# Kernel optimization log

Measured on AMD Instinct MI355X. Metric: run time of the kernel, lower is better.

Reference implementation:

```python
import jax, jax.numpy as jnp
import numpy as np
from jax import lax

DN = ('NCHW', 'OIHW', 'NCHW')

def _pconv(x, mask, w, b):
    # Partial conv: conv(masked x) rescaled by K/valid_count; mask_next = valid>0.
    C = x.shape[1]
    k = w.shape[2]
    p = k // 2
    K = C * k * k
    xm = x * mask  # mask broadcasts over channels (== repeat in torch code)
    xp = jnp.pad(xm, ((0, 0), (0, 0), (p, p), (p, p)))  # zeros, as in F.pad value=0
    y = lax.conv_general_dilated(xp, w, (1, 1), 'VALID', dimension_numbers=DN)
    # mask padded with 1.0 (as in the torch module), summed over kxk window
    mp = jnp.pad(mask, ((0, 0), (0, 0), (p, p), (p, p)), constant_values=1.0)
    ones_k = jnp.ones((1, 1, k, k), x.dtype)
    msum = lax.conv_general_dilated(mp, ones_k, (1, 1), 'VALID', dimension_numbers=DN)
    valid = C * msum  # [N,1,H,W] = sum over all K unfold rows
    scale = K / jnp.maximum(valid, 1.0)
    y = y * scale + b[None, :, None, None]
    no_valid = valid <= 0.0
    y = jnp.where(no_valid, 0.0, y)
    mask_next = (~no_valid).astype(x.dtype)
    return y, mask_next

def _bn_relu(x, gamma, beta, eps=1e-5):
    # training-mode BatchNorm2d: per-batch biased stats over (N,H,W)
    mu = jnp.mean(x, axis=(0, 2, 3), keepdims=True)
    var = jnp.var(x, axis=(0, 2, 3), keepdims=True)
    xn = (x - mu) * lax.rsqrt(var + eps)
    return jax.nn.relu(xn * gamma[None, :, None, None] + beta[None, :, None, None])

def _pool21(x):
    # MaxPool2d(kernel=(2,1), stride=(2,1))
    N, C, H, W = x.shape
    return x.reshape(N, C, H // 2, 2, W).max(axis=3)

def setup_inputs() -> dict:
    key = jax.random.key(0)
    ks = iter(jax.random.split(key, 32))
    base = 80
    def kaiming(k, shape):
        fan_in = shape[1] * shape[2] * shape[3]
        return jax.random.normal(k, shape, jnp.float32) * np.sqrt(2.0 / fan_in)
    def lin(k, out, inp):
        bound = 1.0 / np.sqrt(inp)
        kw, kb = jax.random.split(k)
        W = jax.random.uniform(kw, (out, inp), jnp.float32, -bound, bound)
        b = jax.random.uniform(kb, (out,), jnp.float32, -bound, bound)
        return W, b
    x = jax.random.normal(next(ks), (16, 2, 256, 128), jnp.float32)
    d = {'x': x}
    chans = [(1, base), (base, 2 * base), (2 * base, 4 * base), (4 * base, 8 * base)]
    for i, (ci, co) in enumerate(chans, 1):
        d[f'w{i}'] = kaiming(next(ks), (co, ci, 3, 3))
        d[f'b{i}'] = jnp.zeros((co,), jnp.float32)
        d[f'g{i}'] = jnp.ones((co,), jnp.float32)
        d[f'be{i}'] = jnp.zeros((co,), jnp.float32)
    d['fw1'], d['fb1'] = lin(next(ks), 256, 8 * base)
    d['fw2'], d['fb2'] = lin(next(ks), 128, 256)
    d['hw'], d['hb'] = lin(next(ks), 1, 128)
    return d

def reference(x, w1, b1, g1, be1, w2, b2, g2, be2, w3, b3, g3, be3,
              w4, b4, g4, be4, fw1, fb1, fw2, fb2, hw, hb):
    data = x[:, 0:1, :, :]
    mask = jnp.clip(x[:, 1:2, :, :], 0.0, 1.0)
    h, m = data, mask
    for w, b, g, be in ((w1, b1, g1, be1), (w2, b2, g2, be2),
                        (w3, b3, g3, be3), (w4, b4, g4, be4)):
        h, m = _pconv(h, m, w, b)
        h = _bn_relu(h, g, be)
        h = _pool21(h)
        m = _pool21(m)
    feat = jnp.mean(h, axis=(2, 3))  # GAP -> [N, 8*base]
    z = jax.nn.relu(feat @ fw1.T + fb1)
    z = jax.nn.relu(z @ fw2.T + fb2)  # dropout = identity (eval)
    return jax.nn.sigmoid(z @ hw.T + hb)[:, 0]
```

## Files before the change

### kernel.cpp

```cpp
#include <hip/hip_runtime.h>
#include <math.h>

#define NB 16
#define WD 128

typedef __bf16 bf16_t;
typedef __bf16 bf16x8 __attribute__((ext_vector_type(8)));
typedef __bf16 bf16x4 __attribute__((ext_vector_type(4)));
typedef float f32x4 __attribute__((ext_vector_type(4)));

__device__ inline float rowsum16(float v) {
  int t;
  t = __builtin_amdgcn_update_dpp(0, __float_as_int(v), 0x111, 0xf, 0xf, true);
  v += __int_as_float(t);
  t = __builtin_amdgcn_update_dpp(0, __float_as_int(v), 0x112, 0xf, 0xf, true);
  v += __int_as_float(t);
  t = __builtin_amdgcn_update_dpp(0, __float_as_int(v), 0x114, 0xf, 0xf, true);
  v += __int_as_float(t);
  t = __builtin_amdgcn_update_dpp(0, __float_as_int(v), 0x118, 0xf, 0xf, true);
  v += __int_as_float(t);
  return v;
}

__global__ void zero_k(float* __restrict__ p, int n) {
  int i = blockIdx.x * 256 + threadIdx.x;
  if (i < n) p[i] = 0.f;
}

__global__ void zb_k(bf16_t* __restrict__ out, int Hp, int NCB) {
  int trow = NB * 2 * NCB * 576;
  int tcol = NB * Hp * NCB * 8;
  int i = blockIdx.x * 256 + threadIdx.x;
  bf16x8 z = (bf16x8)(bf16_t)0.f;
  if (i < trow) {
    int e = i % 576;
    int t = i / 576;
    int cb = t % NCB;
    t /= NCB;
    int rsel = t & 1;
    int n = t >> 1;
    int row = rsel ? (Hp + 1) : 0;
    *(bf16x8*)&out[(((size_t)n * (Hp + 2) + row) * NCB + cb) * 4608 + e * 8] = z;
  } else if (i < trow + tcol) {
    int k = i - trow;
    int j = k & 7;
    int t = k >> 3;
    int cb = t % NCB;
    t /= NCB;
    int row = (t % Hp) + 1;
    int n = t / Hp;
    size_t base = (((size_t)n * (Hp + 2) + row) * NCB + cb) * 4608;
    size_t off = (j < 4) ? (size_t)(j * 128) : (size_t)(4096 + (j - 4) * 128 + 8);
    *(bf16x8*)&out[base + off] = z;
  }
}

__global__ void split_k(const float* __restrict__ x, float* __restrict__ data,
                        float* __restrict__ mask) {
  const int HW = 256 * 128;
  int i = blockIdx.x * 256 + threadIdx.x;
  if (i >= NB * HW) return;
  int n = i / HW, rem = i % HW;
  data[i] = x[(size_t)(n * 2) * HW + rem];
  float mv = x[(size_t)(n * 2 + 1) * HW + rem];
  mask[i] = fminf(fmaxf(mv, 0.f), 1.f);
}

__global__ void maskscale2_k(const float* __restrict__ m, float* __restrict__ scale,
                             float* __restrict__ mnext, float* __restrict__ mpool,
                             int H, float Ci) {
  int Hp = H / 2;
  int i = blockIdx.x * 256 + threadIdx.x;
  int tot = NB * Hp * WD;
  if (i >= tot) return;
  int x = i % WD;
  int t = i / WD;
  int yo = t % Hp;
  int n = t / Hp;
  const float* mn_ = m + (size_t)n * H * WD;
  float mx[2];
#pragma unroll
  for (int r = 0; r < 2; ++r) {
    int y = 2 * yo + r;
    float s = 0.f;
#pragma unroll
    for (int dy = -1; dy <= 1; dy++) {
      int yy = y + dy;
#pragma unroll
      for (int dx = -1; dx <= 1; dx++) {
        int xx = x + dx;
        float v = 1.0f;
        if (yy >= 0 && yy < H && xx >= 0 && xx < WD) v = mn_[yy * WD + xx];
        s += v;
      }
    }
    float valid = Ci * s;
    int p = (n * H + y) * WD + x;
    scale[p] = (9.0f * Ci) / fmaxf(valid, 1.0f);
    float mnx = (valid <= 0.0f) ? 0.f : 1.f;
    mnext[p] = mnx;
    mx[r] = mnx;
  }
  mpool[((size_t)n * Hp + yo) * WD + x] = fmaxf(mx[0], mx[1]);
}

__global__ void pconv1_k(const float* __restrict__ data, const float* __restrict__ mask,
                         const float* __restrict__ w, const float* __restrict__ b,
                         const float* __restrict__ scale, const float* __restrict__ mnext,
                         bf16_t* __restrict__ y) {
  __shared__ float ws[720];
  __shared__ float bs[80];
  for (int i = threadIdx.x; i < 720; i += 256) ws[i] = w[i];
  if (threadIdx.x < 80) bs[threadIdx.x] = b[threadIdx.x];
  __syncthreads();
  const int H = 256;
  int p = blockIdx.x * 256 + threadIdx.x;
  int x = p % WD;
  int t = p / WD;
  int yy = t % H;
  int n = t / H;
  const float* dn = data + (size_t)n * H * WD;
  const float* mn = mask + (size_t)n * H * WD;
  float v[9];
#pragma unroll
  for (int dy = 0; dy < 3; dy++) {
    int yv = yy - 1 + dy;
#pragma unroll
    for (int dx = 0; dx < 3; dx++) {
      int xv = x - 1 + dx;
      float u = 0.f;
      if (yv >= 0 && yv < H && xv >= 0 && xv < WD)
        u = dn[yv * WD + xv] * mn[yv * WD + xv];
      v[dy * 3 + dx] = u;
    }
  }
  float sc = scale[p], mx = mnext[p];
  bf16_t* yp = y + (size_t)p * 80;
#pragma unroll
  for (int c8 = 0; c8 < 10; ++c8) {
    bf16x8 o;
#pragma unroll
    for (int j = 0; j < 8; ++j) {
      int co = c8 * 8 + j;
      float s = 0.f;
#pragma unroll
      for (int tt = 0; tt < 9; ++tt) s += ws[co * 9 + tt] * v[tt];
      o[j] = (bf16_t)((s * sc + bs[co]) * mx);
    }
    *(bf16x8*)(yp + c8 * 8) = o;
  }
}

__global__ __launch_bounds__(320) void bnstats_g(const bf16_t* __restrict__ y,
                                                 float* __restrict__ sums, int nc8) {
  const int ITER = 64;
  const int tid = threadIdx.x;
  const int C = nc8 * 8;
  float s[8], q[8];
#pragma unroll
  for (int j = 0; j < 8; ++j) { s[j] = 0.f; q[j] = 0.f; }
  size_t base = (size_t)blockIdx.x * 320 * ITER;
  for (int k = 0; k < ITER; ++k) {
    size_t chunk = base + (size_t)k * 320 + tid;
    bf16x8 v = *(const bf16x8*)(y + chunk * 8);
#pragma unroll
    for (int j = 0; j < 8; ++j) {
      float f = (float)v[j];
      s[j] += f;
      q[j] += f * f;
    }
  }
  __shared__ float red[320][8];
  const int rows = 320 / nc8;
  float ssum[2], qsum[2];
#pragma unroll
  for (int j = 0; j < 8; ++j) red[tid][j] = s[j];
  __syncthreads();
  {
    int idx = 0;
    for (int c = tid; c < C; c += 320, ++idx) {
      int c8 = c >> 3, j = c & 7;
      float acc = 0.f;
      for (int i = 0; i < rows; ++i) acc += red[c8 + nc8 * i][j];
      ssum[idx] = acc;
    }
  }
  __syncthreads();
#pragma unroll
  for (int j = 0; j < 8; ++j) red[tid][j] = q[j];
  __syncthreads();
  {
    int idx = 0;
    for (int c = tid; c < C; c += 320, ++idx) {
      int c8 = c >> 3, j = c & 7;
      float acc = 0.f;
      for (int i = 0; i < rows; ++i) acc += red[c8 + nc8 * i][j];
      qsum[idx] = acc;
      atomicAdd(&sums[c], ssum[idx]);
      atomicAdd(&sums[C + c], qsum[idx]);
    }
  }
}

__global__ void wtrans_k(const float* __restrict__ w, bf16_t* __restrict__ wt2,
                         int Ci, int Co, int NCB, int Co_pad) {
  int idx = blockIdx.x * 256 + threadIdx.x;
  int total = 9 * NCB * Co_pad * 32;
  if (idx >= total) return;
  int j = idx & 7;
  int rest = idx >> 3;
  int co = rest % Co_pad;
  int rest2 = rest / Co_pad;
  int g = rest2 & 3;
  int rest3 = rest2 >> 2;
  int cb = rest3 % NCB;
  int tap = rest3 / NCB;
  int ci = cb * 32 + g * 8 + j;
  float v = 0.f;
  if (co < Co && ci < Ci) v = w[((size_t)co * Ci + ci) * 9 + tap];
  wt2[idx] = (bf16_t)v;
}

#define PROWS 2048
#define PCO 640
template <int MF>
__global__ __launch_bounds__(256, 2) void convmfma_t(
    const bf16_t* __restrict__ xmT, const bf16_t* __restrict__ wt2,
    const float* __restrict__ bias, const float* __restrict__ scale,
    const float* __restrict__ mnext, bf16_t* __restrict__ y,
    float* __restrict__ part, int H, int NCB, int Co, int Cop, int coOff) {
  __shared__ bf16_t Bb[2][4][4608];
  const int tid = threadIdx.x;
  const int lane = tid & 63;
  const int wave = tid >> 6;
  const int wm = wave >> 1;
  const int wn = wave & 1;
  const int g = lane >> 4;
  const int ln = lane & 15;
  constexpr int TILE = MF * 32;
  constexpr int EPS = TILE + 8;
  constexpr int NCO8 = TILE / 8;

  const int gx = gridDim.x;
  const int nwg = gx * (int)gridDim.y;
  const int orig = (int)blockIdx.y * gx + (int)blockIdx.x;
  const int wg = (orig & 7) * (nwg >> 3) + (orig >> 3);
  const int coTile = coOff + (wg % gx) * TILE;
  const int bx = wg / gx;
  const int Hh = H >> 1;
  const int n = bx / Hh, y0 = (bx % Hh) * 2;

  f32x4 acc[MF][8];
#pragma unroll
  for (int mf = 0; mf < MF; mf++)
#pragma unroll
    for (int nf = 0; nf < 8; nf++) acc[mf][nf] = (f32x4)(0.f);

  const size_t cbStride = 4608;
  const size_t rowStrideG = (size_t)NCB * cbStride;
  const size_t gRow0 = ((size_t)n * (H + 2) + y0) * rowStrideG;
  const size_t laneOff = (size_t)lane * 8;

  const size_t tapStrideA = (size_t)NCB * 4 * Cop * 8;
  const size_t cbStrideA = (size_t)4 * Cop * 8;
  const bf16_t* aLane = wt2 + ((size_t)g * Cop + coTile + wm * (MF * 16) + ln) * 8;

  int offdx[3];
#pragma unroll
  for (int dx = 0; dx < 3; ++dx) {
    int cx = ln + dx;
    offdx[dx] = ((cx & 15) * 8) + ((cx >> 4) * 512) + g * 128;
  }

  {
    const bf16_t* bsrc = xmT + gRow0;
    for (int c = wave; c < 36; c += 4) {
      int row = c / 9, chk = c - row * 9;
      __builtin_amdgcn_global_load_lds(
          (const __attribute__((address_space(1))) void*)(
              bsrc + (size_t)row * rowStrideG + chk * 512 + laneOff),
          (__attribute__((address_space(3))) void*)(&Bb[0][row][chk * 512]), 16, 0, 0);
    }
  }
  __syncthreads();

  int cur = 0;
  for (int cb = 0; cb < NCB; ++cb) {
    if (cb + 1 < NCB) {
      const bf16_t* bsrc = xmT + gRow0 + (size_t)(cb + 1) * cbStride;
      for (int c = wave; c < 36; c += 4) {
        int row = c / 9, chk = c - row * 9;
        __builtin_amdgcn_global_load_lds(
            (const __attribute__((address_space(1))) void*)(
                bsrc + (size_t)row * rowStrideG + chk * 512 + laneOff),
            (__attribute__((address_space(3))) void*)(&Bb[cur ^ 1][row][chk * 512]), 16,
            0, 0);
      }
    }
    const bf16_t* aCb = aLane + (size_t)cb * cbStrideA;
#pragma unroll
    for (int dy = 0; dy < 3; ++dy) {
      const bf16_t* brow = &Bb[cur][wn + dy][0];
#pragma unroll
      for (int dx = 0; dx < 3; ++dx) {
        const bf16_t* aTap = aCb + (size_t)(dy * 3 + dx) * tapStrideA;
        bf16x8 a[MF];
#pragma unroll
        for (int mf = 0; mf < MF; ++mf) a[mf] = *(const bf16x8*)(aTap + mf * 128);
        const bf16_t* bb = brow + offdx[dx];
#pragma unroll
        for (int nf = 0; nf < 8; ++nf) {
          bf16x8 b = *(const bf16x8*)(bb + nf * 512);
#pragma unroll
          for (int mf = 0; mf < MF; ++mf)
            acc[mf][nf] =
                __builtin_amdgcn_mfma_f32_16x16x32_bf16(a[mf], b, acc[mf][nf], 0, 0, 0);
        }
      }
    }
    __syncthreads();
    cur ^= 1;
  }

  const int yrowW = y0 + wn;
  const int pixBaseW = (n * H + yrowW) * WD;
  float scl[8], msk[8];
#pragma unroll
  for (int nf = 0; nf < 8; ++nf) {
    int x = nf * 16 + ln;
    scl[nf] = scale[pixBaseW + x];
    msk[nf] = mnext[pixBaseW + x];
  }
  float sA[4 * MF], qA[4 * MF];
#pragma unroll
  for (int i = 0; i < 4 * MF; ++i) { sA[i] = 0.f; qA[i] = 0.f; }
  bf16_t* ep = &Bb[0][0][0];
#pragma unroll
  for (int rp = 0; rp < 2; ++rp) {
    __syncthreads();
    if (wn == rp) {
#pragma unroll
      for (int mf = 0; mf < MF; ++mf) {
        int cbase = wm * (MF * 16) + mf * 16;
        if (coTile + cbase < Co) {
          f32x4 bias4 = *(const f32x4*)&bias[coTile + cbase + g * 4];
#pragma unroll
          for (int nf = 0; nf < 8; ++nf) {
            bf16x4 o;
#pragma unroll
            for (int r = 0; r < 4; ++r) {
              o[r] = (bf16_t)((acc[mf][nf][r] * scl[nf] + bias4[r]) * msk[nf]);
              float f = (float)o[r];
              sA[mf * 4 + r] += f;
              qA[mf * 4 + r] += f * f;
            }
            *(bf16x4*)&ep[(nf * 16 + ln) * EPS + cbase + g * 4] = o;
          }
        }
      }
    }
    __syncthreads();
    const int prow = (n * H + y0 + rp) * WD;
    for (int idx = tid; idx < 128 * NCO8; idx += 256) {
      int cgrp = idx % NCO8;
      int p = idx / NCO8;
      bf16x8 v = *(const bf16x8*)&ep[p * EPS + cgrp * 8];
      *(bf16x8*)&y[(size_t)(prow + p) * Co + coTile + cgrp * 8] = v;
    }
  }

#pragma unroll
  for (int i = 0; i < 4 * MF; ++i) {
    sA[i] = rowsum16(sA[i]);
    qA[i] = rowsum16(qA[i]);
  }
  if (ln == 15) {
    const int row = bx * 2 + wn;
#pragma unroll
    for (int i = 0; i < 4 * MF; ++i) {
      int co = coTile + wm * (MF * 16) + (i >> 2) * 16 + g * 4 + (i & 3);
      part[(size_t)co * PROWS + row] = sA[i];
      part[(size_t)PCO * PROWS + (size_t)co * PROWS + row] = qA[i];
    }
  }
}

__global__ __launch_bounds__(256) void bnfin_r(const float* __restrict__ part,
                                               const float* __restrict__ g,
                                               const float* __restrict__ be,
                                               float* __restrict__ ab, int Co,
                                               int rows, float invCount) {
  int c = blockIdx.x;
  int tid = threadIdx.x;
  float s = 0.f, q = 0.f;
  for (int r = tid; r < rows; r += 256) {
    s += part[(size_t)c * PROWS + r];
    q += part[(size_t)PCO * PROWS + (size_t)c * PROWS + r];
  }
  __shared__ float rs[256], rq[256];
  rs[tid] = s;
  rq[tid] = q;
  __syncthreads();
  for (int off = 128; off > 0; off >>= 1) {
    if (tid < off) {
      rs[tid] += rs[tid + off];
      rq[tid] += rq[tid + off];
    }
    __syncthreads();
  }
  if (tid == 0) {
    float mean = rs[0] * invCount;
    float var = rq[0] * invCount - mean * mean;
    float rsq = rsqrtf(var + 1e-5f);
    float a = g[c] * rsq;
    ab[c] = a;
    ab[Co + c] = be[c] - mean * a;
  }
}

__global__ void bnfin_k(const float* __restrict__ sums, const float* __restrict__ g,
                        const float* __restrict__ be, float* __restrict__ ab, int Co,
                        float invCount) {
  int c = blockIdx.x * 64 + threadIdx.x;
  if (c >= Co) return;
  float mean = sums[c] * invCount;
  float var = sums[Co + c] * invCount - mean * mean;
  float rs = rsqrtf(var + 1e-5f);
  float a = g[c] * rs;
  ab[c] = a;
  ab[Co + c] = be[c] - mean * a;
}

__global__ void bnpool_k(const bf16_t* __restrict__ y, const float* __restrict__ ab,
                         const float* __restrict__ mp, bf16_t* __restrict__ out, int C,
                         int NCBn, int H) {
  int Hp = H / 2;
  int Cq = C / 8;
  int tid = blockIdx.x * 256 + threadIdx.x;
  int total = NB * Hp * WD * Cq;
  if (tid >= total) return;
  int c8 = tid % Cq;
  int t = tid / Cq;
  int x = t % WD;
  t /= WD;
  int yo = t % Hp;
  int n = t / Hp;
  int c = c8 * 8;
  const bf16_t* p0 = y + ((size_t)((n * H + 2 * yo) * WD + x)) * C + c;
  const bf16_t* p1 = p0 + (size_t)WD * C;
  float mpv = mp[(n * Hp + yo) * WD + x];
  bf16x8 v0 = *(const bf16x8*)p0;
  bf16x8 v1 = *(const bf16x8*)p1;
  bf16x8 o;
#pragma unroll
  for (int j = 0; j < 8; ++j) {
    float a = ab[c + j], sh = ab[C + c + j];
    float f0 = (float)v0[j] * a + sh;
    float f1 = (float)v1[j] * a + sh;
    o[j] = (bf16_t)(fmaxf(fmaxf(f0, f1), 0.f) * mpv);
  }
  int cb = c >> 5;
  int gg = (c & 31) >> 3;
  int col = x + 1;
  int chk = col >> 4, lcol = col & 15;
  *(bf16x8*)&out[((((size_t)n * (Hp + 2) + yo + 1) * NCBn + cb) * 9 + chk) * 512 +
                 gg * 128 + lcol * 8] = o;
}

__global__ void bnfeat_k(const bf16_t* __restrict__ y, const float* __restrict__ ab,
                         float* __restrict__ feat) {
  int n = blockIdx.x, cc = blockIdx.y, yo = blockIdx.z;
  int c = cc * 128 + threadIdx.x;
  float a = ab[c], sh = ab[640 + c];
  float s = 0.f;
  for (int x = 0; x < WD; ++x) {
    size_t p0 = ((size_t)(n * 32 + 2 * yo) * WD + x) * 640 + c;
    float v0 = (float)y[p0] * a + sh;
    float v1 = (float)y[p0 + (size_t)WD * 640] * a + sh;
    s += fmaxf(fmaxf(v0, v1), 0.f);
  }
  atomicAdd(&feat[n * 640 + c], s * (1.f / 2048.f));
}

__global__ void fc1_k(const float* __restrict__ feat, const float* __restrict__ fw,
                      const float* __restrict__ fb, float* __restrict__ z1) {
  int n = blockIdx.x;
  int o = threadIdx.x;
  const float* f = feat + n * 640;
  const float* wr = fw + o * 640;
  float s = fb[o];
  for (int k = 0; k < 640; k++) s += f[k] * wr[k];
  z1[n * 256 + o] = fmaxf(s, 0.f);
}

__global__ void fc2h_k(const float* __restrict__ z1, const float* __restrict__ fw2,
                       const float* __restrict__ fb2, const float* __restrict__ hw,
                       const float* __restrict__ hb, float* __restrict__ out) {
  int n = blockIdx.x;
  int o = threadIdx.x;
  const float* zr = z1 + n * 256;
  const float* wr = fw2 + o * 256;
  float s = fb2[o];
  for (int k = 0; k < 256; k++) s += zr[k] * wr[k];
  s = fmaxf(s, 0.f) * hw[o];
#pragma unroll
  for (int off = 32; off >= 1; off >>= 1) s += __shfl_down(s, off, 64);
  __shared__ float red[2];
  if ((threadIdx.x & 63) == 0) red[threadIdx.x >> 6] = s;
  __syncthreads();
  if (threadIdx.x == 0) {
    float t = red[0] + red[1] + hb[0];
    out[n] = 1.f / (1.f + expf(-t));
  }
}

extern "C" void kernel_launch(void* const* d_in, const int* in_sizes, int n_in,
                              void* d_out, int out_size, void* d_ws, size_t ws_size,
                              hipStream_t stream) {
  const float* x = (const float*)d_in[0];
  const float* wgt[4] = {(const float*)d_in[1], (const float*)d_in[5],
                         (const float*)d_in[9], (const float*)d_in[13]};
  const float* bias[4] = {(const float*)d_in[2], (const float*)d_in[6],
                          (const float*)d_in[10], (const float*)d_in[14]};
  const float* gam[4] = {(const float*)d_in[3], (const float*)d_in[7],
                         (const float*)d_in[11], (const float*)d_in[15]};
  const float* bet[4] = {(const float*)d_in[4], (const float*)d_in[8],
                         (const float*)d_in[12], (const float*)d_in[16]};
  const float* fw1 = (const float*)d_in[17];
  const float* fb1 = (const float*)d_in[18];
  const float* fw2 = (const float*)d_in[19];
  const float* fb2 = (const float*)d_in[20];
  const float* hw = (const float*)d_in[21];
  const float* hb = (const float*)d_in[22];

  char* base = (char*)d_ws;
  size_t off = 0;
  auto alloc = [&](size_t bytes) {
    char* p = base + off;
    off += (bytes + 255) & ~(size_t)255;
    return p;
  };
  bf16_t* bufY = (bf16_t*)alloc(83886080);
  const size_t xmtElems = 28786688;
  bf16_t* xmT0 = (bf16_t*)alloc(xmtElems * 2);
  bf16_t* xmT1 = (bf16_t*)alloc(xmtElems * 2);
  bf16_t* wt2 = (bf16_t*)alloc(3686400);
  float* data = (float*)alloc(2097152);
  float* mask0 = (float*)alloc(2097152);
  float* mask1 = (float*)alloc(2097152);
  float* scaleB = (float*)alloc(2097152);
  float* mnextB = (float*)alloc(2097152);
  float* part = (float*)alloc(2 * 640 * 2048 * 4);
  float* sums = (float*)alloc(5120);
  float* bnab = (float*)alloc(5120);
  float* feat = (float*)alloc(40960);
  float* z1 = (float*)alloc(16384);

  zero_k<<<40, 256, 0, stream>>>(feat, 10240);

  split_k<<<(NB * 256 * 128 + 255) / 256, 256, 0, stream>>>(x, data, mask0);

  {
    int H = 256;
    int tot = NB * H * WD;
    maskscale2_k<<<(tot / 2 + 255) / 256, 256, 0, stream>>>(mask0, scaleB, mnextB,
                                                            mask1, H, 1.0f);
    zero_k<<<1, 256, 0, stream>>>(sums, 160);
    pconv1_k<<<tot / 256, 256, 0, stream>>>(data, mask0, wgt[0], bias[0], scaleB,
                                            mnextB, bufY);
    bnstats_g<<<256, 320, 0, stream>>>(bufY, sums, 10);
    bnfin_k<<<2, 64, 0, stream>>>(sums, gam[0], bet[0], bnab, 80,
                                  1.0f / (NB * (float)H * WD));
    {
      int tz = NB * 2 * 3 * 576 + NB * 128 * 3 * 8;
      zb_k<<<(tz + 255) / 256, 256, 0, stream>>>(xmT0, 128, 3);
    }
    int totp = NB * (H / 2) * WD * (80 / 8);
    bnpool_k<<<(totp + 255) / 256, 256, 0, stream>>>(bufY, bnab, mask1, xmT0, 80, 3, H);
  }

  const int CiS[3] = {80, 160, 320};
  const int NCBS[3] = {3, 5, 10};
  const int CoS[3] = {160, 320, 640};
  const int HS[3] = {128, 64, 32};
  bf16_t* xin[3] = {xmT0, xmT1, xmT0};
  bf16_t* xout[3] = {xmT1, xmT0, nullptr};
  float* mIn[3] = {mask1, mask0, mask1};
  float* mOut[3] = {mask0, mask1, mask0 };

  for (int s = 0; s < 3; ++s) {
    int H = HS[s], Ci = CiS[s], NCB = NCBS[s], Co = CoS[s];
    int wtot = 9 * NCB * Co * 32;
    wtrans_k<<<(wtot + 255) / 256, 256, 0, stream>>>(wgt[s + 1], wt2, Ci, Co, NCB, Co);
    int tot = NB * H * WD;
    maskscale2_k<<<(tot / 2 + 255) / 256, 256, 0, stream>>>(mIn[s], scaleB, mnextB,
                                                            mOut[s], H, (float)Ci);
    int Hh2 = NB * (H / 2);
    int tiles = Co / 160;
    convmfma_t<5><<<dim3(tiles, Hh2), 256, 0, stream>>>(
        xin[s], wt2, bias[s + 1], scaleB, mnextB, bufY, part, H, NCB, Co, Co, 0);
    bnfin_r<<<Co, 256, 0, stream>>>(part, gam[s + 1], bet[s + 1], bnab, Co, NB * H,
                                    1.0f / (NB * (float)H * WD));
    if (s < 2) {
      int Hpn = H / 2, NCBn = NCBS[s + 1];
      int tz = NB * 2 * NCBn * 576 + NB * Hpn * NCBn * 8;
      zb_k<<<(tz + 255) / 256, 256, 0, stream>>>(xout[s], Hpn, NCBn);
      int totp = NB * (H / 2) * WD * (Co / 8);
      bnpool_k<<<(totp + 255) / 256, 256, 0, stream>>>(bufY, bnab, mOut[s], xout[s], Co,
                                                       NCBn, H);
    } else {
      bnfeat_k<<<dim3(16, 5, 16), 128, 0, stream>>>(bufY, bnab, feat);
    }
  }

  fc1_k<<<16, 256, 0, stream>>>(feat, fw1, fb1, z1);
  fc2h_k<<<16, 128, 0, stream>>>(z1, fw2, fb2, hw, hb, (float*)d_out);
}
```

Before: 711.6 us.

## Switch conv implicit GEMM to 32x32x16 MFMA with restructured wave tiling

Replaces the 16x16x32 bf16 MFMA tiling with 32x32x16 MFMA instructions. Each wave now covers all 160 output channels (5 tiles) over 64 pixels instead of splitting channels between waves. The point is to cut LDS B-fragment loads and the instruction count per FLOP. The epilogue is reworked for the 32x32 accumulator layout: the BN partial sums are reduced with a cross-row DPP and written at per-wave granularity, so the partial buffer rows double. The trade-offs are more register pressure from the 160 accumulator floats and more partial-stat writes.

```diff
diff --git a/kernel.cpp b/kernel.cpp
--- a/kernel.cpp
+++ b/kernel.cpp
@@ -8,6 +8,7 @@
 typedef __bf16 bf16x8 __attribute__((ext_vector_type(8)));
 typedef __bf16 bf16x4 __attribute__((ext_vector_type(4)));
 typedef float f32x4 __attribute__((ext_vector_type(4)));
+typedef float f32x16 __attribute__((ext_vector_type(16)));
 
 __device__ inline float rowsum16(float v) {
   int t;
@@ -20,6 +21,12 @@
   t = __builtin_amdgcn_update_dpp(0, __float_as_int(v), 0x118, 0xf, 0xf, true);
   v += __int_as_float(t);
   return v;
+}
+
+__device__ inline float colsum32(float v) {
+  v = rowsum16(v);
+  int t = __builtin_amdgcn_update_dpp(0, __float_as_int(v), 0x142, 0xf, 0xf, true);
+  return v + __int_as_float(t);
 }
 
 __global__ void zero_k(float* __restrict__ p, int n) {
@@ -221,23 +228,23 @@
   wt2[idx] = (bf16_t)v;
 }
 
-#define PROWS 2048
+#define PROWS 4096
 #define PCO 640
-template <int MF>
-__global__ __launch_bounds__(256, 2) void convmfma_t(
+__global__ __launch_bounds__(256, 2) void convmfma32_k(
     const bf16_t* __restrict__ xmT, const bf16_t* __restrict__ wt2,
     const float* __restrict__ bias, const float* __restrict__ scale,
     const float* __restrict__ mnext, bf16_t* __restrict__ y,
-    float* __restrict__ part, int H, int NCB, int Co, int Cop, int coOff) {
+    float* __restrict__ part, int H, int NCB, int Co) {
   __shared__ bf16_t Bb[2][4][4608];
   const int tid = threadIdx.x;
   const int lane = tid & 63;
   const int wave = tid >> 6;
-  const int wm = wave >> 1;
   const int wn = wave & 1;
-  const int g = lane >> 4;
-  const int ln = lane & 15;
-  constexpr int TILE = MF * 32;
+  const int wp = wave >> 1;
+  const int half = lane >> 5;
+  const int l31 = lane & 31;
+  constexpr int TILE = 160;
+  constexpr int NT = 5;
   constexpr int EPS = TILE + 8;
   constexpr int NCO8 = TILE / 8;
 
@@ -245,32 +252,34 @@
   const int nwg = gx * (int)gridDim.y;
   const int orig = (int)blockIdx.y * gx + (int)blockIdx.x;
   const int wg = (orig & 7) * (nwg >> 3) + (orig >> 3);
-  const int coTile = coOff + (wg % gx) * TILE;
+  const int coTile = (wg % gx) * TILE;
   const int bx = wg / gx;
   const int Hh = H >> 1;
   const int n = bx / Hh, y0 = (bx % Hh) * 2;
 
-  f32x4 acc[MF][8];
-#pragma unroll
-  for (int mf = 0; mf < MF; mf++)
-#pragma unroll
-    for (int nf = 0; nf < 8; nf++) acc[mf][nf] = (f32x4)(0.f);
+  f32x16 acc[NT][2];
+#pragma unroll
+  for (int t5 = 0; t5 < NT; t5++)
+#pragma unroll
+    for (int pt = 0; pt < 2; pt++) acc[t5][pt] = (f32x16)(0.f);
 
   const size_t cbStride = 4608;
   const size_t rowStrideG = (size_t)NCB * cbStride;
   const size_t gRow0 = ((size_t)n * (H + 2) + y0) * rowStrideG;
   const size_t laneOff = (size_t)lane * 8;
 
-  const size_t tapStrideA = (size_t)NCB * 4 * Cop * 8;
-  const size_t cbStrideA = (size_t)4 * Cop * 8;
-  const bf16_t* aLane = wt2 + ((size_t)g * Cop + coTile + wm * (MF * 16) + ln) * 8;
-
-  int offdx[3];
+  const size_t tapStrideA = (size_t)NCB * 4 * Co * 8;
+  const size_t cbStrideA = (size_t)4 * Co * 8;
+  const size_t sStrideA = (size_t)2 * Co * 8;
+  const bf16_t* aLane = wt2 + ((size_t)half * Co + coTile + l31) * 8;
+
+  int offd[3];
 #pragma unroll
   for (int dx = 0; dx < 3; ++dx) {
-    int cx = ln + dx;
-    offdx[dx] = ((cx & 15) * 8) + ((cx >> 4) * 512) + g * 128;
-  }
+    int c32 = l31 + dx;
+    offd[dx] = ((c32 & 15) * 8) + ((c32 >> 4) * 512) + half * 128;
+  }
+  const int pxOff = wp * 2048;
 
   {
     const bf16_t* bsrc = xmT + gRow0;
@@ -304,17 +313,20 @@
 #pragma unroll
       for (int dx = 0; dx < 3; ++dx) {
         const bf16_t* aTap = aCb + (size_t)(dy * 3 + dx) * tapStrideA;
-        bf16x8 a[MF];
-#pragma unroll
-        for (int mf = 0; mf < MF; ++mf) a[mf] = *(const bf16x8*)(aTap + mf * 128);
-        const bf16_t* bb = brow + offdx[dx];
-#pragma unroll
-        for (int nf = 0; nf < 8; ++nf) {
-          bf16x8 b = *(const bf16x8*)(bb + nf * 512);
-#pragma unroll
-          for (int mf = 0; mf < MF; ++mf)
-            acc[mf][nf] =
-                __builtin_amdgcn_mfma_f32_16x16x32_bf16(a[mf], b, acc[mf][nf], 0, 0, 0);
+#pragma unroll
+        for (int s = 0; s < 2; ++s) {
+          const bf16_t* bb = brow + pxOff + s * 256 + offd[dx];
+          bf16x8 b0 = *(const bf16x8*)(bb);
+          bf16x8 b1 = *(const bf16x8*)(bb + 1024);
+          const bf16_t* aS = aTap + (size_t)s * sStrideA;
+#pragma unroll
+          for (int t5 = 0; t5 < NT; ++t5) {
+            bf16x8 a = *(const bf16x8*)(aS + t5 * 256);
+            acc[t5][0] =
+                __builtin_amdgcn_mfma_f32_32x32x16_bf16(a, b0, acc[t5][0], 0, 0, 0);
+            acc[t5][1] =
+                __builtin_amdgcn_mfma_f32_32x32x16_bf16(a, b1, acc[t5][1], 0, 0, 0);
+          }
         }
       }
     }
@@ -324,37 +336,52 @@
 
   const int yrowW = y0 + wn;
   const int pixBaseW = (n * H + yrowW) * WD;
-  float scl[8], msk[8];
-#pragma unroll
-  for (int nf = 0; nf < 8; ++nf) {
-    int x = nf * 16 + ln;
-    scl[nf] = scale[pixBaseW + x];
-    msk[nf] = mnext[pixBaseW + x];
-  }
-  float sA[4 * MF], qA[4 * MF];
-#pragma unroll
-  for (int i = 0; i < 4 * MF; ++i) { sA[i] = 0.f; qA[i] = 0.f; }
+  float scl[2], msk[2];
+#pragma unroll
+  for (int pt = 0; pt < 2; ++pt) {
+    int x = wp * 64 + pt * 32 + l31;
+    scl[pt] = scale[pixBaseW + x];
+    msk[pt] = mnext[pixBaseW + x];
+  }
   bf16_t* ep = &Bb[0][0][0];
+  const int prowRow = bx * 4 + wn * 2 + wp;
 #pragma unroll
   for (int rp = 0; rp < 2; ++rp) {
     __syncthreads();
     if (wn == rp) {
 #pragma unroll
-      for (int mf = 0; mf < MF; ++mf) {
-        int cbase = wm * (MF * 16) + mf * 16;
-        if (coTile + cbase < Co) {
-          f32x4 bias4 = *(const f32x4*)&bias[coTile + cbase + g * 4];
-#pragma unroll
-          for (int nf = 0; nf < 8; ++nf) {
+      for (int t5 = 0; t5 < NT; ++t5) {
+        float s16[16], q16[16];
+#pragma unroll
+        for (int i = 0; i < 16; ++i) { s16[i] = 0.f; q16[i] = 0.f; }
+#pragma unroll
+        for (int q = 0; q < 4; ++q) {
+          f32x4 bias4 = *(const f32x4*)&bias[coTile + t5 * 32 + q * 8 + half * 4];
+#pragma unroll
+          for (int pt = 0; pt < 2; ++pt) {
             bf16x4 o;
 #pragma unroll
             for (int r = 0; r < 4; ++r) {
-              o[r] = (bf16_t)((acc[mf][nf][r] * scl[nf] + bias4[r]) * msk[nf]);
+              o[r] = (bf16_t)((acc[t5][pt][q * 4 + r] * scl[pt] + bias4[r]) * msk[pt]);
               float f = (float)o[r];
-              sA[mf * 4 + r] += f;
-              qA[mf * 4 + r] += f * f;
+              s16[q * 4 + r] += f;
+              q16[q * 4 + r] += f * f;
             }
-            *(bf16x4*)&ep[(nf * 16 + ln) * EPS + cbase + g * 4] = o;
+            *(bf16x4*)&ep[(wp * 64 + pt * 32 + l31) * EPS + t5 * 32 + q * 8 +
+                          half * 4] = o;
+          }
+        }
+#pragma unroll
+        for (int i = 0; i < 16; ++i) {
+          s16[i] = colsum32(s16[i]);
+          q16[i] = colsum32(q16[i]);
+        }
+        if (l31 == 31) {
+#pragma unroll
+          for (int i = 0; i < 16; ++i) {
+            int co = coTile + t5 * 32 + (i >> 2) * 8 + half * 4 + (i & 3);
+            part[(size_t)co * PROWS + prowRow] = s16[i];
+            part[(size_t)PCO * PROWS + (size_t)co * PROWS + prowRow] = q16[i];
           }
         }
       }
@@ -366,21 +393,6 @@
       int p = idx / NCO8;
       bf16x8 v = *(const bf16x8*)&ep[p * EPS + cgrp * 8];
       *(bf16x8*)&y[(size_t)(prow + p) * Co + coTile + cgrp * 8] = v;
-    }
-  }
-
-#pragma unroll
-  for (int i = 0; i < 4 * MF; ++i) {
-    sA[i] = rowsum16(sA[i]);
-    qA[i] = rowsum16(qA[i]);
-  }
-  if (ln == 15) {
-    const int row = bx * 2 + wn;
-#pragma unroll
-    for (int i = 0; i < 4 * MF; ++i) {
-      int co = coTile + wm * (MF * 16) + (i >> 2) * 16 + g * 4 + (i & 3);
-      part[(size_t)co * PROWS + row] = sA[i];
-      part[(size_t)PCO * PROWS + (size_t)co * PROWS + row] = qA[i];
     }
   }
 }
@@ -550,7 +562,7 @@
   float* mask1 = (float*)alloc(2097152);
   float* scaleB = (float*)alloc(2097152);
   float* mnextB = (float*)alloc(2097152);
-  float* part = (float*)alloc(2 * 640 * 2048 * 4);
+  float* part = (float*)alloc((size_t)2 * 640 * 4096 * 4);
   float* sums = (float*)alloc(5120);
   float* bnab = (float*)alloc(5120);
   float* feat = (float*)alloc(40960);
@@ -597,10 +609,10 @@
                                                             mOut[s], H, (float)Ci);
     int Hh2 = NB * (H / 2);
     int tiles = Co / 160;
-    convmfma_t<5><<<dim3(tiles, Hh2), 256, 0, stream>>>(
-        xin[s], wt2, bias[s + 1], scaleB, mnextB, bufY, part, H, NCB, Co, Co, 0);
-    bnfin_r<<<Co, 256, 0, stream>>>(part, gam[s + 1], bet[s + 1], bnab, Co, NB * H,
-                                    1.0f / (NB * (float)H * WD));
+    convmfma32_k<<<dim3(tiles, Hh2), 256, 0, stream>>>(
+        xin[s], wt2, bias[s + 1], scaleB, mnextB, bufY, part, H, NCB, Co);
+    bnfin_r<<<Co, 256, 0, stream>>>(part, gam[s + 1], bet[s + 1], bnab, Co,
+                                    NB * H * 2, 1.0f / (NB * (float)H * WD));
     if (s < 2) {
       int Hpn = H / 2, NCBn = NCBS[s + 1];
       int tz = NB * 2 * NCBn * 576 + NB * Hpn * NCBn * 8;
```

New measurement: 1.016 ms. +42.8%, slower.
